# Kernel tuning notes

Measured on AMD Instinct MI355X. Metric: run time of the kernel, lower is better.

The kernel has to match this reference:

```python
import jax, jax.numpy as jnp
import numpy as np

D_MODEL = 1024
D_STATE = 16
DT_RANK = 64  # ceil(1024/16)
DT_MIN, DT_MAX = 1e-3, 1e-1


def setup_inputs() -> dict:
    key = jax.random.key(0)
    ks = jax.random.split(key, 6)
    x = jax.random.normal(ks[0], (2, 2048, D_MODEL), jnp.float32)
    A_log = jax.random.normal(ks[1], (D_MODEL, D_STATE), jnp.float32)
    D = jax.random.normal(ks[2], (D_MODEL,), jnp.float32)
    # nn.Linear default init ~ U(-1/sqrt(fan_in), 1/sqrt(fan_in)); normal*scale is fine for a baseline
    x_proj_w = jax.random.normal(ks[3], (DT_RANK + 2 * D_STATE, D_MODEL), jnp.float32) * (D_MODEL ** -0.5)
    dt_init_std = DT_RANK ** -0.5
    dt_proj_w = jax.random.uniform(ks[4], (D_MODEL, DT_RANK), jnp.float32, -dt_init_std, dt_init_std)
    dt = jnp.exp(jax.random.uniform(ks[5], (D_MODEL,), jnp.float32)
                 * (np.log(DT_MAX) - np.log(DT_MIN)) + np.log(DT_MIN))
    dt_proj_b = dt + jnp.log(-jnp.expm1(-dt))  # inverse-softplus init
    return {"x": x, "A_log": A_log, "D": D, "x_proj_w": x_proj_w,
            "dt_proj_w": dt_proj_w, "dt_proj_b": dt_proj_b}


def _s6(x, A_log, D, x_proj_w, dt_proj_w, dt_proj_b):
    A = -jnp.exp(A_log)                                    # (d, n)
    xp = jnp.einsum('bld,ed->ble', x, x_proj_w)            # (b, l, r+2n)
    d_rank = xp[..., :DT_RANK]
    Bm = xp[..., DT_RANK:DT_RANK + D_STATE]                # (b, l, n)
    Cm = xp[..., DT_RANK + D_STATE:]                       # (b, l, n)
    delta = jax.nn.softplus(jnp.einsum('blr,dr->bld', d_rank, dt_proj_w) + dt_proj_b)
    deltaA = jnp.exp(jnp.einsum('bld,dn->bldn', delta, A))          # (b, l, d, n)
    deltaB_u = jnp.einsum('bld,bln,bld->bldn', delta, Bm, x)        # (b, l, d, n)

    def step(h, inp):
        dA_t, dBu_t, C_t = inp          # (b,d,n), (b,d,n), (b,n)
        h = dA_t * h + dBu_t
        y = jnp.einsum('bdn,bn->bd', h, C_t)
        return h, y

    b, l, d = x.shape
    h0 = jnp.zeros((b, d, D_STATE), x.dtype)
    _, ys = jax.lax.scan(step, h0,
                         (deltaA.transpose(1, 0, 2, 3),
                          deltaB_u.transpose(1, 0, 2, 3),
                          Cm.transpose(1, 0, 2)))
    y = ys.transpose(1, 0, 2) + x * D                      # (b, l, d)
    return y


def reference(x, A_log, D, x_proj_w, dt_proj_w, dt_proj_b):
    return _s6(x, A_log, D, x_proj_w, dt_proj_w, dt_proj_b)
```

## Files before the change

kernel.cpp:

```cpp
#include <hip/hip_runtime.h>
#include <math.h>

#define Bb 2
#define Ll 2048
#define Dm 1024
#define Ns 16
#define Rr 64
#define Ee 96
#define BLK (Bb*Ll)
#define NTHR 256
#define LOG2E 1.4426950408889634f
#define LN2   0.6931471805599453f

typedef __attribute__((ext_vector_type(8))) short bf16x8;
typedef __attribute__((ext_vector_type(4))) float f32x4;

__device__ inline float ex2(float x) {
#if __has_builtin(__builtin_amdgcn_exp2f)
    return __builtin_amdgcn_exp2f(x);
#else
    return exp2f(x);
#endif
}
__device__ inline float lg2(float x) {
#if __has_builtin(__builtin_amdgcn_logf)
    return __builtin_amdgcn_logf(x);
#else
    return log2f(x);
#endif
}
__device__ inline float softplus_f(float z) {
    float e = ex2(-fabsf(z) * LOG2E);
    return fmaxf(z, 0.f) + lg2(1.f + e) * LN2;
}

__device__ inline unsigned short f2bf(float f) {
    union { float f; unsigned u; } v; v.f = f;
    unsigned u = v.u + 0x7fffu + ((v.u >> 16) & 1u);
    return (unsigned short)(u >> 16);
}
__device__ inline uint2 pack4(float a, float b, float c, float d) {
    unsigned u0 = ((unsigned)f2bf(b) << 16) | f2bf(a);
    unsigned u1 = ((unsigned)f2bf(d) << 16) | f2bf(c);
    return make_uint2(u0, u1);
}

__global__ void __launch_bounds__(NTHR)
k_xproj(const float* __restrict__ x, const float* __restrict__ xw,
        float* __restrict__ xp) {
    __shared__ __align__(16) short sm[4 * 7168];
    int tid = threadIdx.x;
    int lane = tid & 63, wid = tid >> 6;
    int i0 = blockIdx.x * 16;
    short* wA = sm + wid * 7168;
    short* wB = wA + 1024;

    f32x4 acc[6];
#pragma unroll
    for (int t = 0; t < 6; ++t) acc[t] = (f32x4)0.f;
    int ra = lane & 15;

    for (int ch = 0; ch < 4; ++ch) {
        int kb = wid * 256 + ch * 64;
#pragma unroll
        for (int i = 0; i < 4; ++i) {
            int idx = lane + i * 64;
            int r = idx >> 4, c4 = idx & 15;
            float4 v = *(const float4*)(x + (size_t)(i0 + r) * Dm + kb + c4 * 4);
            int unit = (c4 >> 1) ^ (r & 7);
            *(uint2*)(wA + r * 64 + unit * 8 + (c4 & 1) * 4) = pack4(v.x, v.y, v.z, v.w);
        }
#pragma unroll
        for (int i = 0; i < 24; ++i) {
            int idx = lane + i * 64;
            int r = idx >> 4, c4 = idx & 15;
            float4 v = *(const float4*)(xw + (size_t)r * Dm + kb + c4 * 4);
            int unit = (c4 >> 1) ^ (r & 7);
            *(uint2*)(wB + r * 64 + unit * 8 + (c4 & 1) * 4) = pack4(v.x, v.y, v.z, v.w);
        }
#pragma unroll
        for (int ks = 0; ks < 2; ++ks) {
            int g = ks * 4 + (lane >> 4);
            bf16x8 a = *(bf16x8*)(wA + ra * 64 + ((g ^ (ra & 7)) << 3));
#pragma unroll
            for (int nt = 0; nt < 6; ++nt) {
                int br = nt * 16 + (lane & 15);
                bf16x8 b = *(bf16x8*)(wB + br * 64 + ((g ^ (br & 7)) << 3));
                acc[nt] = __builtin_amdgcn_mfma_f32_16x16x32_bf16(a, b, acc[nt], 0, 0, 0);
            }
        }
    }
    __syncthreads();
    float* rp = (float*)sm;
#pragma unroll
    for (int nt = 0; nt < 6; ++nt)
#pragma unroll
        for (int j = 0; j < 4; ++j) {
            int r = ((lane >> 4) << 2) + j;
            int c = nt * 16 + (lane & 15);
            rp[wid * 1536 + r * 96 + c] = acc[nt][j];
        }
    __syncthreads();
#pragma unroll
    for (int o = 0; o < 6; ++o) {
        int idx = o * 256 + tid;
        float s = rp[idx] + rp[1536 + idx] + rp[3072 + idx] + rp[4608 + idx];
        int r = idx / 96, c = idx - r * 96;
        xp[(size_t)(i0 + r) * Ee + c] = s;
    }
}

__global__ void __launch_bounds__(NTHR)
k_delta(const float* __restrict__ xp, const float* __restrict__ dtw,
        const float* __restrict__ dtb, float* __restrict__ delta) {
    __shared__ __align__(16) short sA[128 * 64];
    __shared__ __align__(16) short sB[64 * 64];
    int tid = threadIdx.x, lane = tid & 63, wid = tid >> 6;
    int nt16 = blockIdx.x & 15, mt = blockIdx.x >> 4;
    int i0 = mt * 128, j0 = nt16 * 64;

#pragma unroll
    for (int i = 0; i < 8; ++i) {
        int idx = tid + i * 256;
        int r = idx >> 4, c4 = idx & 15;
        float4 v = *(const float4*)(xp + (size_t)(i0 + r) * Ee + c4 * 4);
        int unit = (c4 >> 1) ^ (r & 7);
        *(uint2*)(sA + r * 64 + unit * 8 + (c4 & 1) * 4) = pack4(v.x, v.y, v.z, v.w);
    }
#pragma unroll
    for (int i = 0; i < 4; ++i) {
        int idx = tid + i * 256;
        int r = idx >> 4, c4 = idx & 15;
        float4 v = *(const float4*)(dtw + (size_t)(j0 + r) * Rr + c4 * 4);
        int unit = (c4 >> 1) ^ (r & 7);
        *(uint2*)(sB + r * 64 + unit * 8 + (c4 & 1) * 4) = pack4(v.x, v.y, v.z, v.w);
    }
    __syncthreads();

    f32x4 acc[2][4];
#pragma unroll
    for (int m = 0; m < 2; ++m)
#pragma unroll
        for (int nt = 0; nt < 4; ++nt) acc[m][nt] = (f32x4)0.f;
    int R = wid * 32;
    int r0 = R + (lane & 15), r1 = R + 16 + (lane & 15);
#pragma unroll
    for (int ks = 0; ks < 2; ++ks) {
        int g = ks * 4 + (lane >> 4);
        bf16x8 a0 = *(bf16x8*)(sA + r0 * 64 + ((g ^ (r0 & 7)) << 3));
        bf16x8 a1 = *(bf16x8*)(sA + r1 * 64 + ((g ^ (r1 & 7)) << 3));
#pragma unroll
        for (int nt = 0; nt < 4; ++nt) {
            int br = nt * 16 + (lane & 15);
            bf16x8 b = *(bf16x8*)(sB + br * 64 + ((g ^ (br & 7)) << 3));
            acc[0][nt] = __builtin_amdgcn_mfma_f32_16x16x32_bf16(a0, b, acc[0][nt], 0, 0, 0);
            acc[1][nt] = __builtin_amdgcn_mfma_f32_16x16x32_bf16(a1, b, acc[1][nt], 0, 0, 0);
        }
    }
#pragma unroll
    for (int nt = 0; nt < 4; ++nt) {
        int col = j0 + nt * 16 + (lane & 15);
        float bias = dtb[col];
#pragma unroll
        for (int m = 0; m < 2; ++m)
#pragma unroll
            for (int j = 0; j < 4; ++j) {
                int row = i0 + R + m * 16 + ((lane >> 4) << 2) + j;
                delta[(size_t)row * Dm + col] = softplus_f(acc[m][nt][j] + bias);
            }
    }
}

__device__ inline void load_a2(const float* __restrict__ A_log, int d, float* a2) {
    const float4* Ap = (const float4*)(A_log + (size_t)d * Ns);
    float4 a0 = Ap[0], a1 = Ap[1], a2v = Ap[2], a3 = Ap[3];
    float tmp[Ns] = {a0.x,a0.y,a0.z,a0.w, a1.x,a1.y,a1.z,a1.w,
                     a2v.x,a2v.y,a2v.z,a2v.w, a3.x,a3.y,a3.z,a3.w};
#pragma unroll
    for (int n = 0; n < Ns; ++n) a2[n] = -__expf(tmp[n]) * LOG2E;
}

template<int CHv>
__global__ void __launch_bounds__(NTHR)
k_scan_part(const float* __restrict__ delta, const float* __restrict__ x,
            const float* __restrict__ xp, const float* __restrict__ A_log,
            float* __restrict__ Ec, float* __restrict__ Sc) {
    constexpr int CLv = Ll / CHv;
    int bx = blockIdx.x;
    int dblk = bx & 3, chunk = (bx >> 2) & (CHv - 1), b = bx >> 2 >> __builtin_ctz(CHv);
    int tid = threadIdx.x;
    int d = dblk * 256 + tid;
    int row0 = b * Ll + chunk * CLv;

    float a2[Ns], h[Ns];
    load_a2(A_log, d, a2);
#pragma unroll
    for (int n = 0; n < Ns; ++n) h[n] = 0.f;
    float sd = 0.f;

#pragma unroll 4
    for (int t = 0; t < CLv; ++t) {
        size_t row = (size_t)(row0 + t);
        float dl = delta[row * Dm + d];
        float xv = x[row * Dm + d];
        const float* bp = xp + row * Ee + Rr;
        float4 B0 = *(const float4*)(bp + 0),  B1 = *(const float4*)(bp + 4);
        float4 B2 = *(const float4*)(bp + 8),  B3 = *(const float4*)(bp + 12);
        float Bv[Ns] = {B0.x,B0.y,B0.z,B0.w, B1.x,B1.y,B1.z,B1.w,
                        B2.x,B2.y,B2.z,B2.w, B3.x,B3.y,B3.z,B3.w};
        float dx = dl * xv;
        sd += dl;
#pragma unroll
        for (int n = 0; n < Ns; ++n)
            h[n] = fmaf(ex2(dl * a2[n]), h[n], dx * Bv[n]);
    }
    size_t base = ((size_t)b * CHv + chunk) * Dm + d;
    float4* Ep = (float4*)(Ec + base * Ns);
    Ep[0] = make_float4(h[0],  h[1],  h[2],  h[3]);
    Ep[1] = make_float4(h[4],  h[5],  h[6],  h[7]);
    Ep[2] = make_float4(h[8],  h[9],  h[10], h[11]);
    Ep[3] = make_float4(h[12], h[13], h[14], h[15]);
    Sc[base] = sd;
}

template<int CHv, int G>
__global__ void __launch_bounds__(NTHR)
k_comb1(const float* __restrict__ Ec, const float* __restrict__ Sc,
        const float* __restrict__ A_log, float* __restrict__ Hloc,
        float* __restrict__ Spre, float* __restrict__ Eg, float* __restrict__ Sg) {
    constexpr int CPG = CHv / G;
    int gid = blockIdx.x * NTHR + threadIdx.x;
    int n = gid & (Ns - 1);
    int d = (gid >> 4) & (Dm - 1);
    int g = (gid >> 14) & (G - 1);
    int b = gid >> 17;
    float a2 = -__expf(A_log[d * Ns + n]) * LOG2E;
    float h = 0.f, S = 0.f;
#pragma unroll
    for (int j = 0; j < CPG; ++j) {
        size_t base = ((size_t)b * CHv + g * CPG + j) * Dm + d;
        float e  = Ec[base * Ns + n];
        float sc = Sc[base];
        Hloc[base * Ns + n] = h;
        if (n == 0) Spre[base] = S;
        h = fmaf(ex2(a2 * sc), h, e);
        S += sc;
    }
    size_t gb = ((size_t)b * G + g) * Dm + d;
    Eg[gb * Ns + n] = h;
    if (n == 0) Sg[gb] = S;
}

template<int G>
__global__ void __launch_bounds__(NTHR)
k_comb2(const float* __restrict__ Eg, const float* __restrict__ Sg,
        const float* __restrict__ A_log, float* __restrict__ Hg) {
    int gid = blockIdx.x * NTHR + threadIdx.x;
    int n = gid & (Ns - 1);
    int d = (gid >> 4) & (Dm - 1);
    int b = gid >> 14;
    float a2 = -__expf(A_log[d * Ns + n]) * LOG2E;
    float h = 0.f;
#pragma unroll
    for (int g = 0; g < G; ++g) {
        size_t gb = ((size_t)b * G + g) * Dm + d;
        Hg[gb * Ns + n] = h;
        h = fmaf(ex2(a2 * Sg[gb]), h, Eg[gb * Ns + n]);
    }
}

template<int CHv, int G>
__global__ void __launch_bounds__(NTHR)
k_scan_full(const float* __restrict__ delta, const float* __restrict__ x,
            const float* __restrict__ xp, const float* __restrict__ A_log,
            const float* __restrict__ Dp, const float* __restrict__ Hloc,
            const float* __restrict__ Spre, const float* __restrict__ Hg,
            float* __restrict__ out) {
    constexpr int CLv = Ll / CHv;
    constexpr int CPG = CHv / G;
    int bx = blockIdx.x;
    int dblk = bx & 3, chunk = (bx >> 2) & (CHv - 1), b = bx >> 2 >> __builtin_ctz(CHv);
    int tid = threadIdx.x;
    int d = dblk * 256 + tid;
    int row0 = b * Ll + chunk * CLv;

    float a2[Ns], h[Ns];
    load_a2(A_log, d, a2);
    size_t base = ((size_t)b * CHv + chunk) * Dm + d;
    size_t gb   = ((size_t)b * G + chunk / CPG) * Dm + d;
    {
        float sp = Spre[base];
        const float4* Hl = (const float4*)(Hloc + base * Ns);
        const float4* Hp = (const float4*)(Hg + gb * Ns);
        float4 l0 = Hl[0], l1 = Hl[1], l2 = Hl[2], l3 = Hl[3];
        float4 g0 = Hp[0], g1 = Hp[1], g2 = Hp[2], g3 = Hp[3];
        float lv[Ns] = {l0.x,l0.y,l0.z,l0.w, l1.x,l1.y,l1.z,l1.w,
                        l2.x,l2.y,l2.z,l2.w, l3.x,l3.y,l3.z,l3.w};
        float gv[Ns] = {g0.x,g0.y,g0.z,g0.w, g1.x,g1.y,g1.z,g1.w,
                        g2.x,g2.y,g2.z,g2.w, g3.x,g3.y,g3.z,g3.w};
#pragma unroll
        for (int n = 0; n < Ns; ++n) h[n] = fmaf(ex2(a2[n] * sp), gv[n], lv[n]);
    }
    float Dval = Dp[d];

#pragma unroll 4
    for (int t = 0; t < CLv; ++t) {
        size_t row = (size_t)(row0 + t);
        float dl = delta[row * Dm + d];
        float xv = x[row * Dm + d];
        const float* bp = xp + row * Ee + Rr;
        float4 B0 = *(const float4*)(bp + 0),  B1 = *(const float4*)(bp + 4);
        float4 B2 = *(const float4*)(bp + 8),  B3 = *(const float4*)(bp + 12);
        float4 C0 = *(const float4*)(bp + 16), C1 = *(const float4*)(bp + 20);
        float4 C2 = *(const float4*)(bp + 24), C3 = *(const float4*)(bp + 28);
        float Bv[Ns] = {B0.x,B0.y,B0.z,B0.w, B1.x,B1.y,B1.z,B1.w,
                        B2.x,B2.y,B2.z,B2.w, B3.x,B3.y,B3.z,B3.w};
        float Cv[Ns] = {C0.x,C0.y,C0.z,C0.w, C1.x,C1.y,C1.z,C1.w,
                        C2.x,C2.y,C2.z,C2.w, C3.x,C3.y,C3.z,C3.w};
        float dx = dl * xv;
        float ya[4] = {0.f, 0.f, 0.f, 0.f};
#pragma unroll
        for (int n = 0; n < Ns; ++n) {
            h[n] = fmaf(ex2(dl * a2[n]), h[n], dx * Bv[n]);
            ya[n & 3] = fmaf(h[n], Cv[n], ya[n & 3]);
        }
        out[row * Dm + d] = fmaf(xv, Dval, (ya[0] + ya[1]) + (ya[2] + ya[3]));
    }
}

extern "C" void kernel_launch(void* const* d_in, const int* in_sizes, int n_in,
                              void* d_out, int out_size, void* d_ws, size_t ws_size,
                              hipStream_t stream) {
    const float* x     = (const float*)d_in[0];
    const float* A_log = (const float*)d_in[1];
    const float* Dp    = (const float*)d_in[2];
    const float* xw    = (const float*)d_in[3];
    const float* dtw   = (const float*)d_in[4];
    const float* dtb   = (const float*)d_in[5];
    float* out = (float*)d_out;
    float* ws  = (float*)d_ws;

    float* xp    = ws;
    float* delta = xp + 393216;
    float* S3    = delta + 4194304;

    k_xproj<<<dim3(256), dim3(NTHR), 0, stream>>>(x, xw, xp);
    k_delta<<<dim3(512), dim3(NTHR), 0, stream>>>(xp, dtw, dtb, delta);

    constexpr int G = 8;
    constexpr int CHv = 64;
    float* Ec   = S3;
    float* Sc   = Ec   + (size_t)Bb*CHv*Dm*Ns;
    float* Hloc = Sc   + (size_t)Bb*CHv*Dm;
    float* Spre = Hloc + (size_t)Bb*CHv*Dm*Ns;
    float* Eg   = Spre + (size_t)Bb*CHv*Dm;
    float* Sg   = Eg   + (size_t)Bb*G*Dm*Ns;
    float* Hg   = Sg   + (size_t)Bb*G*Dm;

    k_scan_part<CHv>  <<<dim3(Bb*CHv*4), dim3(NTHR), 0, stream>>>(delta, x, xp, A_log, Ec, Sc);
    k_comb1<CHv, G>   <<<dim3(Bb*G*Dm*Ns/NTHR), dim3(NTHR), 0, stream>>>(Ec, Sc, A_log, Hloc, Spre, Eg, Sg);
    k_comb2<G>        <<<dim3(Bb*Dm*Ns/NTHR), dim3(NTHR), 0, stream>>>(Eg, Sg, A_log, Hg);
    k_scan_full<CHv,G><<<dim3(Bb*CHv*4), dim3(NTHR), 0, stream>>>(delta, x, xp, A_log, Dp, Hloc, Spre, Hg, out);
}
```

Before: 163.2 us.

## Share x_proj LDS tiles across warps with block-cooperative loads and smaller footprint

The x projection kernel previously gave each of the four warps its own private 7168-short LDS region covering a separate quarter of the K dimension. It now uses a single shared A/B tile of 128 columns per chunk, loaded by all 256 threads, with each warp taking one 32-wide K slice for its MFMAs. LDS use drops from about 57 KB to about 28 KB, and launch bounds now request 4 blocks per CU so more blocks can be resident. In exchange it adds two __syncthreads per chunk across 8 chunks, and the load/compute phases are still not overlapped.

```diff
diff --git a/kernel.cpp b/kernel.cpp
--- a/kernel.cpp
+++ b/kernel.cpp
@@ -45,52 +45,49 @@
     return make_uint2(u0, u1);
 }
 
-__global__ void __launch_bounds__(NTHR)
+__global__ void __launch_bounds__(NTHR, 4)
 k_xproj(const float* __restrict__ x, const float* __restrict__ xw,
         float* __restrict__ xp) {
-    __shared__ __align__(16) short sm[4 * 7168];
-    int tid = threadIdx.x;
-    int lane = tid & 63, wid = tid >> 6;
+    __shared__ __align__(16) short sm[16*128 + 96*128];
+    int tid = threadIdx.x, lane = tid & 63, wid = tid >> 6;
     int i0 = blockIdx.x * 16;
-    short* wA = sm + wid * 7168;
-    short* wB = wA + 1024;
+    short* sA = sm;
+    short* sB = sm + 16*128;
 
     f32x4 acc[6];
 #pragma unroll
     for (int t = 0; t < 6; ++t) acc[t] = (f32x4)0.f;
     int ra = lane & 15;
 
-    for (int ch = 0; ch < 4; ++ch) {
-        int kb = wid * 256 + ch * 64;
-#pragma unroll
-        for (int i = 0; i < 4; ++i) {
-            int idx = lane + i * 64;
-            int r = idx >> 4, c4 = idx & 15;
+    for (int ch = 0; ch < 8; ++ch) {
+        int kb = ch * 128;
+#pragma unroll
+        for (int i = 0; i < 2; ++i) {
+            int idx = tid + i * 256;
+            int r = idx >> 5, c4 = idx & 31;
             float4 v = *(const float4*)(x + (size_t)(i0 + r) * Dm + kb + c4 * 4);
             int unit = (c4 >> 1) ^ (r & 7);
-            *(uint2*)(wA + r * 64 + unit * 8 + (c4 & 1) * 4) = pack4(v.x, v.y, v.z, v.w);
-        }
-#pragma unroll
-        for (int i = 0; i < 24; ++i) {
-            int idx = lane + i * 64;
-            int r = idx >> 4, c4 = idx & 15;
+            *(uint2*)(sA + r * 128 + unit * 8 + (c4 & 1) * 4) = pack4(v.x, v.y, v.z, v.w);
+        }
+#pragma unroll
+        for (int i = 0; i < 12; ++i) {
+            int idx = tid + i * 256;
+            int r = idx >> 5, c4 = idx & 31;
             float4 v = *(const float4*)(xw + (size_t)r * Dm + kb + c4 * 4);
             int unit = (c4 >> 1) ^ (r & 7);
-            *(uint2*)(wB + r * 64 + unit * 8 + (c4 & 1) * 4) = pack4(v.x, v.y, v.z, v.w);
-        }
-#pragma unroll
-        for (int ks = 0; ks < 2; ++ks) {
-            int g = ks * 4 + (lane >> 4);
-            bf16x8 a = *(bf16x8*)(wA + ra * 64 + ((g ^ (ra & 7)) << 3));
-#pragma unroll
-            for (int nt = 0; nt < 6; ++nt) {
-                int br = nt * 16 + (lane & 15);
-                bf16x8 b = *(bf16x8*)(wB + br * 64 + ((g ^ (br & 7)) << 3));
-                acc[nt] = __builtin_amdgcn_mfma_f32_16x16x32_bf16(a, b, acc[nt], 0, 0, 0);
-            }
-        }
-    }
-    __syncthreads();
+            *(uint2*)(sB + r * 128 + unit * 8 + (c4 & 1) * 4) = pack4(v.x, v.y, v.z, v.w);
+        }
+        __syncthreads();
+        int g = wid * 4 + (lane >> 4);
+        bf16x8 a = *(bf16x8*)(sA + ra * 128 + ((g ^ (ra & 7)) << 3));
+#pragma unroll
+        for (int nt = 0; nt < 6; ++nt) {
+            int br = nt * 16 + (lane & 15);
+            bf16x8 b = *(bf16x8*)(sB + br * 128 + ((g ^ (br & 7)) << 3));
+            acc[nt] = __builtin_amdgcn_mfma_f32_16x16x32_bf16(a, b, acc[nt], 0, 0, 0);
+        }
+        __syncthreads();
+    }
     float* rp = (float*)sm;
 #pragma unroll
     for (int nt = 0; nt < 6; ++nt)
```

After: 161.8 us. No clear change (-0.9%).
